# Optimization experiments

Measured on AMD Instinct MI355X. Metric: run time of the kernel, lower is better.

Reference implementation:

```python
import jax, jax.numpy as jnp
import numpy as np

B, L, E = 8, 2048, 128


def setup_inputs() -> dict:
    key = jax.random.key(0)
    k1, k2, k3, k4 = jax.random.split(key, 4)
    return {
        "Uq": jax.random.normal(k1, (B, L, E), dtype=jnp.float32),
        "Uid": jax.random.normal(k2, (B, L, E), dtype=jnp.float32),
        "mask": jnp.ones((L, L), dtype=jnp.float32),
        "Wc_w": jax.random.normal(k3, (3 * E,), dtype=jnp.float32) * 0.05,
        "Wc_b": jax.random.normal(k4, (), dtype=jnp.float32) * 0.05,
    }


def reference(Uq, Uid, mask, Wc_w, Wc_b):
    # Wc(cat(Uid, Uq, Uid*Uq)) decomposed into three direct projections —
    # exact same math as the Linear over the concatenation, never
    # materializing the [B, L, L, 3E] tensor.
    e = Uq.shape[-1]
    w_id, w_q, w_mul = Wc_w[:e], Wc_w[e:2 * e], Wc_w[2 * e:]
    s_id = jnp.einsum("bie,e->bi", Uid, w_id)          # [B, Lid]
    s_q = jnp.einsum("bje,e->bj", Uq, w_q)             # [B, Lq]
    s_mul = jnp.einsum("bie,bje,e->bij", Uid, Uq, w_mul)  # [B, Lid, Lq]
    S = (s_id[:, :, None] + s_q[:, None, :] + s_mul + Wc_b) * mask
    # S_D2Q = Softmax(dim=0) over the per-example [Lid, Lq] matrix -> axis=1
    P = jax.nn.softmax(S, axis=1)                      # [B, Lid, Lq]
    A_D2Q = jnp.einsum("bij,bje->bie", P, Uq)          # [B, Lid, E]
    M = jnp.einsum("bij,bkj->bik", P, P)               # P @ P^T, [B, Lid, Lid]
    A_Q2D = jnp.einsum("bik,bke->bie", M, Uid)         # [B, Lid, E]
    Vid = jnp.concatenate([Uid, A_D2Q, Uid * A_D2Q, Uid * A_Q2D], axis=-1)
    return Vid  # [B, Lid, 4E]
```

## Files before the change

kernel.cpp:

```cpp
#include <hip/hip_runtime.h>

#define L 2048
#define E 128
#define NB 8

typedef float f32x4 __attribute__((ext_vector_type(4)));
typedef short short8 __attribute__((ext_vector_type(8)));
typedef unsigned int u32;

static __device__ inline float bf2f(ushort u) {
  union { float f; u32 i; } v; v.i = ((u32)u) << 16; return v.f;
}
static __device__ inline ushort f2bf(float f) {
  union { float f; u32 i; } v; v.f = f;
  u32 x = v.i;
  return (ushort)((x + 0x7fffu + ((x >> 16) & 1u)) >> 16);
}

__device__ inline void glds16(const ushort* g, ushort* l) {
  __builtin_amdgcn_global_load_lds(
      (const __attribute__((address_space(1))) u32*)(const void*)g,
      (__attribute__((address_space(3))) u32*)(void*)l, 16, 0, 0);
}

__global__ __launch_bounds__(128) void k_prep(const float* __restrict__ Uq,
                                              const float* __restrict__ Uid,
                                              const float* __restrict__ Wcw,
                                              ushort* __restrict__ UqB,
                                              ushort* __restrict__ UidB,
                                              ushort* __restrict__ Uidw,
                                              float* __restrict__ s_id,
                                              float* __restrict__ s_q) {
  int r = blockIdx.x;
  int e = threadIdx.x;
  ushort uqu  = f2bf(Uq[(long)r * E + e]);
  ushort uidu = f2bf(Uid[(long)r * E + e]);
  float uqf = bf2f(uqu), uidf = bf2f(uidu);
  float wid  = bf2f(f2bf(Wcw[e]));
  float wq   = bf2f(f2bf(Wcw[E + e]));
  float wmul = bf2f(f2bf(Wcw[2 * E + e]));
  UqB[(long)r * E + e]  = uqu;
  UidB[(long)r * E + e] = uidu;
  Uidw[(long)r * E + e] = f2bf(uidf * wmul);
  float sid = uidf * wid, sq = uqf * wq;
  #pragma unroll
  for (int off = 32; off >= 1; off >>= 1) {
    sid += __shfl_down(sid, off, 64);
    sq  += __shfl_down(sq,  off, 64);
  }
  __shared__ float red[4];
  int wv = threadIdx.x >> 6;
  if ((threadIdx.x & 63) == 0) { red[wv * 2] = sid; red[wv * 2 + 1] = sq; }
  __syncthreads();
  if (threadIdx.x == 0) { s_id[r] = red[0] + red[2]; s_q[r] = red[1] + red[3]; }
}

__global__ __launch_bounds__(256) void k_maskT(const float* __restrict__ mask,
                                               ushort* __restrict__ maskT) {
  __shared__ ushort tile[32][33];
  int j0 = blockIdx.x * 32, i0 = blockIdx.y * 32;
  int tx = threadIdx.x, ty = threadIdx.y;
  #pragma unroll
  for (int r = ty; r < 32; r += 8)
    tile[r][tx] = f2bf(mask[(long)(i0 + r) * L + j0 + tx]);
  __syncthreads();
  #pragma unroll
  for (int r = ty; r < 32; r += 8)
    maskT[(long)(j0 + r) * L + i0 + tx] = tile[tx][r];
}

__global__ __launch_bounds__(256) void k_tr2(const ushort* __restrict__ s1,
                                             ushort* __restrict__ d1,
                                             const ushort* __restrict__ s2,
                                             ushort* __restrict__ d2) {
  __shared__ ushort tile[32][33];
  int zz = blockIdx.z;
  long base = (long)(zz & (NB - 1)) * L * E;
  const ushort* src = ((zz < NB) ? s1 : s2) + base;
  ushort* dst = ((zz < NB) ? d1 : d2) + base;
  int c0 = blockIdx.x * 32, r0 = blockIdx.y * 32;
  int tx = threadIdx.x, ty = threadIdx.y;
  #pragma unroll
  for (int i = ty; i < 32; i += 8)
    tile[i][tx] = src[(long)(r0 + i) * E + c0 + tx];
  __syncthreads();
  #pragma unroll
  for (int i = ty; i < 32; i += 8)
    dst[(long)(c0 + i) * L + r0 + tx] = tile[tx][i];
}

__device__ inline void gemm128_loop(const ushort* __restrict__ A,
                                    const ushort* __restrict__ B,
                                    long ldA, long ldB, int K,
                                    f32x4 acc[4][4],
                                    ushort* ldsA, ushort* ldsB) {
  const int t = threadIdx.x;
  const int w = t >> 6, lane = t & 63;
  const int mrow = lane & 15, quad = lane >> 4;
  const int lr = lane >> 3;
  const int lc = ((lane & 7) ^ lr) * 8;
  const int mh = (w & 1) * 64, nh = (w >> 1) * 64;
  for (int k0 = 0; k0 < K; k0 += 64) {
    __syncthreads();
    #pragma unroll
    for (int s = 0; s < 4; s++) {
      int row = w * 32 + s * 8 + lr;
      glds16(&A[(long)row * ldA + k0 + lc], &ldsA[w * 2048 + s * 512]);
      glds16(&B[(long)row * ldB + k0 + lc], &ldsB[w * 2048 + s * 512]);
    }
    __syncthreads();
    #pragma unroll
    for (int kk = 0; kk < 2; kk++) {
      short8 av[4], bv[4];
      #pragma unroll
      for (int mi = 0; mi < 4; mi++)
        av[mi] = *(const short8*)&ldsA[(mh + mi * 16 + mrow) * 64 +
                                       ((kk * 32 + quad * 8) ^ ((mrow & 7) << 3))];
      #pragma unroll
      for (int ni = 0; ni < 4; ni++)
        bv[ni] = *(const short8*)&ldsB[(nh + ni * 16 + mrow) * 64 +
                                       ((kk * 32 + quad * 8) ^ ((mrow & 7) << 3))];
      #pragma unroll
      for (int mi = 0; mi < 4; mi++)
        #pragma unroll
        for (int ni = 0; ni < 4; ni++)
          acc[mi][ni] = __builtin_amdgcn_mfma_f32_16x16x32_bf16(av[mi], bv[ni], acc[mi][ni], 0, 0, 0);
    }
  }
}

__device__ inline void gemm64x64_dbuf(const ushort* __restrict__ A,
                                      const ushort* __restrict__ B,
                                      long ldA, long ldB, int K,
                                      f32x4 acc[2][2],
                                      ushort* ldsA, ushort* ldsB) {
  const int t = threadIdx.x;
  const int w = t >> 6, lane = t & 63;
  const int mrow = lane & 15, quad = lane >> 4;
  const int lr = lane >> 3;
  const int lc = ((lane & 7) ^ lr) * 8;
  const int mh = (w & 1) * 32, nh = (w >> 1) * 32;
  #pragma unroll
  for (int s = 0; s < 2; s++) {
    int row = w * 16 + s * 8 + lr;
    glds16(&A[(long)row * ldA + lc], &ldsA[w * 1024 + s * 512]);
    glds16(&B[(long)row * ldB + lc], &ldsB[w * 1024 + s * 512]);
  }
  int cur = 0;
  for (int k0 = 0; k0 < K; k0 += 64) {
    __syncthreads();
    int nxt = cur ^ 1;
    if (k0 + 64 < K) {
      #pragma unroll
      for (int s = 0; s < 2; s++) {
        int row = w * 16 + s * 8 + lr;
        glds16(&A[(long)row * ldA + k0 + 64 + lc], &ldsA[nxt * 4096 + w * 1024 + s * 512]);
        glds16(&B[(long)row * ldB + k0 + 64 + lc], &ldsB[nxt * 4096 + w * 1024 + s * 512]);
      }
    }
    const ushort* cA = &ldsA[cur * 4096];
    const ushort* cB = &ldsB[cur * 4096];
    #pragma unroll
    for (int kk = 0; kk < 2; kk++) {
      short8 av[2], bv[2];
      #pragma unroll
      for (int mi = 0; mi < 2; mi++)
        av[mi] = *(const short8*)&cA[(mh + mi * 16 + mrow) * 64 +
                                     ((kk * 32 + quad * 8) ^ ((mrow & 7) << 3))];
      #pragma unroll
      for (int ni = 0; ni < 2; ni++)
        bv[ni] = *(const short8*)&cB[(nh + ni * 16 + mrow) * 64 +
                                     ((kk * 32 + quad * 8) ^ ((mrow & 7) << 3))];
      #pragma unroll
      for (int mi = 0; mi < 2; mi++)
        #pragma unroll
        for (int ni = 0; ni < 2; ni++)
          acc[mi][ni] = __builtin_amdgcn_mfma_f32_16x16x32_bf16(av[mi], bv[ni], acc[mi][ni], 0, 0, 0);
    }
    cur = nxt;
  }
}

__global__ __launch_bounds__(256) void k_scores(const ushort* __restrict__ Uq,
                                                const ushort* __restrict__ Uidw,
                                                const float* __restrict__ s_id,
                                                const float* __restrict__ s_q,
                                                const float* __restrict__ Wcb,
                                                const ushort* __restrict__ maskT,
                                                ushort* __restrict__ St,
                                                float* __restrict__ ps, int b0) {
  __shared__ ushort lds[16384];
  ushort* ldsA = lds;
  ushort* ldsB = lds + 8192;
  int bz = blockIdx.z, b = b0 + bz;
  int m0 = blockIdx.x * 128;
  int n0 = blockIdx.y * 128;
  int tile_i = blockIdx.y;
  const ushort* A = Uq   + (long)b * L * E + (long)m0 * E;
  const ushort* B = Uidw + (long)b * L * E + (long)n0 * E;
  f32x4 acc[4][4] = {};
  gemm128_loop(A, B, E, E, E, acc, ldsA, ldsB);
  float bias = bf2f(f2bf(Wcb[0]));
  const int t = threadIdx.x, w = t >> 6, lane = t & 63;
  const int col = lane & 15, quad = lane >> 4;
  const int mh = (w & 1) * 64, nh = (w >> 1) * 64;

  __syncthreads();
  float sidv[4];
  #pragma unroll
  for (int ni = 0; ni < 4; ni++)
    sidv[ni] = s_id[b * L + n0 + nh + ni * 16 + col];
  #pragma unroll
  for (int mi = 0; mi < 4; mi++) {
    float sqv[4];
    #pragma unroll
    for (int rg = 0; rg < 4; rg++)
      sqv[rg] = s_q[b * L + m0 + mh + mi * 16 + quad * 4 + rg];
    #pragma unroll
    for (int ni = 0; ni < 4; ni++) {
      int cl = nh + ni * 16 + col;
      #pragma unroll
      for (int rg = 0; rg < 4; rg++) {
        int row = mh + mi * 16 + quad * 4 + rg;
        float v = acc[mi][ni][rg] + sqv[rg] + sidv[ni] + bias;
        lds[row * 128 + (cl ^ ((row & 7) << 3))] = f2bf(v);
      }
    }
  }
  __syncthreads();
  ushort oall[64];
  #pragma unroll
  for (int p = 0; p < 8; p++) {
    int r2 = p * 16 + (t >> 4);
    int cu = (t & 15) * 8;
    uint4 sv = *(const uint4*)&lds[r2 * 128 + (cu ^ ((r2 & 7) << 3))];
    int jg = m0 + r2;
    uint4 mv = *(const uint4*)&maskT[(long)jg * L + n0 + cu];
    float lsum = 0.f;
    const ushort* sp = (const ushort*)&sv;
    const ushort* mp = (const ushort*)&mv;
    #pragma unroll
    for (int k = 0; k < 8; k++) {
      float ev = __expf(bf2f(sp[k]) * bf2f(mp[k]));
      oall[p * 8 + k] = f2bf(ev);
      lsum += bf2f(oall[p * 8 + k]);
    }
    #pragma unroll
    for (int off = 8; off >= 1; off >>= 1) lsum += __shfl_xor(lsum, off, 64);
    if ((t & 15) == 0) {
      ps[((long)bz * L + jg) * 16 + tile_i] = lsum;
    }
  }
  #pragma unroll
  for (int p = 0; p < 8; p++) {
    int r2 = p * 16 + (t >> 4);
    int cu = (t & 15) * 8;
    int jg = m0 + r2;
    *(uint4*)&St[(long)bz * L * L + (long)jg * L + n0 + cu] = *(const uint4*)&oall[p * 8];
  }
}

__global__ __launch_bounds__(256) void k_redstats(const float* __restrict__ ps,
                                                  float* __restrict__ lg) {
  int idx = blockIdx.x * 256 + threadIdx.x;
  const float* psr = ps + (long)idx * 16;
  float s = 0.f;
  #pragma unroll
  for (int k = 0; k < 16; k++) s += psr[k];
  lg[idx] = 1.0f / s;
}

__global__ __launch_bounds__(256) void k_gemm_Tt(const ushort* __restrict__ UidT,
                                                 const ushort* __restrict__ Et,
                                                 const float* __restrict__ lg,
                                                 ushort* __restrict__ Tt, int b0) {
  __shared__ ushort lds[16384];
  ushort* ldsA = lds;
  ushort* ldsB = lds + 8192;
  int bz = blockIdx.z, b = b0 + bz;
  int e0 = (blockIdx.x & 1) * 64;
  int j0 = (blockIdx.x >> 1) * 64;
  const ushort* A = UidT + (long)b * E * L + (long)e0 * L;
  const ushort* B = Et   + (long)bz * L * L + (long)j0 * L;
  f32x4 acc[2][2] = {};
  gemm64x64_dbuf(A, B, L, L, L, acc, ldsA, ldsB);
  const int t = threadIdx.x, w = t >> 6, lane = t & 63;
  const int col = lane & 15, quad = lane >> 4;
  const int mh = (w & 1) * 32, nh = (w >> 1) * 32;
  __syncthreads();
  #pragma unroll
  for (int mi = 0; mi < 2; mi++)
    #pragma unroll
    for (int ni = 0; ni < 2; ni++) {
      int cl = nh + ni * 16 + col;
      float sc = lg[(long)bz * L + j0 + cl];
      #pragma unroll
      for (int rg = 0; rg < 4; rg++) {
        int row = mh + mi * 16 + quad * 4 + rg;
        lds[row * 64 + (cl ^ ((row & 7) << 3))] = f2bf(acc[mi][ni][rg] * sc);
      }
    }
  __syncthreads();
  #pragma unroll
  for (int p = 0; p < 2; p++) {
    int r2 = p * 32 + (t >> 3);
    int cu = (t & 7) * 8;
    uint4 v = *(const uint4*)&lds[r2 * 64 + (cu ^ ((r2 & 7) << 3))];
    *(uint4*)&Tt[(long)b * E * L + (long)(e0 + r2) * L + j0 + cu] = v;
  }
}

__global__ __launch_bounds__(512) void k_gemm_A(const ushort* __restrict__ Et,
                                                const ushort* __restrict__ UqT,
                                                const ushort* __restrict__ Tt,
                                                const ushort* __restrict__ UidB,
                                                const float* __restrict__ lg,
                                                float* __restrict__ out, int b0) {
  __shared__ ushort ldsA[2 * 4608];
  __shared__ ushort ldsB[2 * 8192];
  int bz = blockIdx.z, b = b0 + bz;
  int m0 = blockIdx.x * 64;
  int n0 = blockIdx.y * 128;
  const ushort* Eb = Et + (long)bz * L * L + m0;
  const float* lgb = lg + (long)bz * L;
  const ushort* B = (blockIdx.y == 0) ? (UqT + (long)b * E * L)
                                      : (Tt  + (long)b * E * L);
  const int t = threadIdx.x, w = t >> 6, lane = t & 63;
  const int mrow = lane & 15, quad = lane >> 4;
  const int lr = lane >> 3;
  const int lc = ((lane & 7) ^ lr) * 8;
  const int mh = (w & 1) * 32, nh = (w >> 1) * 32;
  const int jp2 = (t >> 4) * 2;
  const int ic  = (t & 15) * 4;
  f32x4 acc[2][2] = {};
  uint2 q0 = *(const uint2*)&Eb[(long)jp2 * L + ic];
  uint2 q1 = *(const uint2*)&Eb[(long)(jp2 + 1) * L + ic];
  float s0 = lgb[jp2], s1 = lgb[jp2 + 1];
  #pragma unroll
  for (int s = 0; s < 2; s++) {
    int row = w * 16 + s * 8 + lr;
    glds16(&B[(long)row * L + lc], &ldsB[w * 1024 + s * 512]);
  }
  {
    const ushort* p0 = (const ushort*)&q0;
    const ushort* p1 = (const ushort*)&q1;
    #pragma unroll
    for (int k = 0; k < 4; k++) {
      u32 pk = (u32)f2bf(bf2f(p0[k]) * s0) |
               ((u32)f2bf(bf2f(p1[k]) * s1) << 16);
      int i = ic + k;
      int cs = jp2 ^ (((i >> 3) & 7) << 3);
      *(u32*)&ldsA[i * 72 + cs] = pk;
    }
  }
  q0 = *(const uint2*)&Eb[(long)(64 + jp2) * L + ic];
  q1 = *(const uint2*)&Eb[(long)(64 + jp2 + 1) * L + ic];
  s0 = lgb[64 + jp2]; s1 = lgb[64 + jp2 + 1];

  int cur = 0;
  for (int k0 = 0; k0 < L; k0 += 64) {
    __syncthreads();
    int nxt = cur ^ 1;
    if (k0 + 64 < L) {
      #pragma unroll
      for (int s = 0; s < 2; s++) {
        int row = w * 16 + s * 8 + lr;
        glds16(&B[(long)row * L + k0 + 64 + lc], &ldsB[nxt * 8192 + w * 1024 + s * 512]);
      }
      const ushort* p0 = (const ushort*)&q0;
      const ushort* p1 = (const ushort*)&q1;
      #pragma unroll
      for (int k = 0; k < 4; k++) {
        u32 pk = (u32)f2bf(bf2f(p0[k]) * s0) |
                 ((u32)f2bf(bf2f(p1[k]) * s1) << 16);
        int i = ic + k;
        int cs = jp2 ^ (((i >> 3) & 7) << 3);
        *(u32*)&ldsA[nxt * 4608 + i * 72 + cs] = pk;
      }
    }
    if (k0 + 128 < L) {
      q0 = *(const uint2*)&Eb[(long)(k0 + 128 + jp2) * L + ic];
      q1 = *(const uint2*)&Eb[(long)(k0 + 128 + jp2 + 1) * L + ic];
      s0 = lgb[k0 + 128 + jp2]; s1 = lgb[k0 + 128 + jp2 + 1];
    }
    const ushort* cA = &ldsA[cur * 4608];
    const ushort* cB = &ldsB[cur * 8192];
    #pragma unroll
    for (int kk = 0; kk < 2; kk++) {
      short8 av[2], bv[2];
      #pragma unroll
      for (int mi = 0; mi < 2; mi++) {
        int i = mh + mi * 16 + mrow;
        av[mi] = *(const short8*)&cA[i * 72 +
                   ((kk * 32 + quad * 8) ^ (((i >> 3) & 7) << 3))];
      }
      #pragma unroll
      for (int ni = 0; ni < 2; ni++)
        bv[ni] = *(const short8*)&cB[(nh + ni * 16 + mrow) * 64 +
                                     ((kk * 32 + quad * 8) ^ ((mrow & 7) << 3))];
      #pragma unroll
      for (int mi = 0; mi < 2; mi++)
        #pragma unroll
        for (int ni = 0; ni < 2; ni++)
          acc[mi][ni] = __builtin_amdgcn_mfma_f32_16x16x32_bf16(av[mi], bv[ni], acc[mi][ni], 0, 0, 0);
    }
    cur = nxt;
  }
  const int col = mrow;
  #pragma unroll
  for (int mi = 0; mi < 2; mi++)
    #pragma unroll
    for (int ni = 0; ni < 2; ni++)
      #pragma unroll
      for (int rg = 0; rg < 4; rg++) {
        int ig = m0 + mh + mi * 16 + quad * 4 + rg;
        int c  = n0 + nh + ni * 16 + col;
        float a = acc[mi][ni][rg];
        float uidf = bf2f(UidB[(long)b * L * E + (long)ig * E + (c & 127)]);
        long ob = ((long)b * L + ig) * 512;
        if (c < 128) {
          out[ob + c]       = uidf;
          out[ob + 128 + c] = a;
          out[ob + 256 + c] = uidf * a;
        } else {
          out[ob + 256 + c] = uidf * a;
        }
      }
}

extern "C" void kernel_launch(void* const* d_in, const int* in_sizes, int n_in,
                              void* d_out, int out_size, void* d_ws, size_t ws_size,
                              hipStream_t stream) {
  const float* Uq   = (const float*)d_in[0];
  const float* Uid  = (const float*)d_in[1];
  const float* mask = (const float*)d_in[2];
  const float* Wcw  = (const float*)d_in[3];
  const float* Wcb  = (const float*)d_in[4];
  float* out = (float*)d_out;

  char* ws = (char*)d_ws;
  size_t off = 0;
  auto alloc = [&](size_t bytes) -> void* {
    void* p = ws + off; off += (bytes + 255) & ~(size_t)255; return p;
  };
  const size_t nUb = (size_t)NB * L * E * 2;
  ushort* UqB   = (ushort*)alloc(nUb);
  ushort* UidB  = (ushort*)alloc(nUb);
  ushort* Uidw  = (ushort*)alloc(nUb);
  ushort* UqT   = (ushort*)alloc(nUb);
  ushort* UidT  = (ushort*)alloc(nUb);
  ushort* Tt    = (ushort*)alloc(nUb);
  ushort* maskT = (ushort*)alloc((size_t)L * L * 2);
  float*  s_id  = (float*)alloc((size_t)NB * L * 4);
  float*  s_q   = (float*)alloc((size_t)NB * L * 4);
  float*  lg    = (float*)alloc((size_t)NB * L * 4);
  float*  ps    = (float*)alloc((size_t)NB * L * 16 * 4);
  const size_t per_batch = (size_t)L * L * 2;
  size_t avail = (ws_size > off + per_batch) ? (ws_size - off) : per_batch;
  int nb_c = (int)(avail / per_batch);
  if (nb_c < 1) nb_c = 1;
  if (nb_c > NB) nb_c = NB;
  ushort* St = (ushort*)(ws + off);

  dim3 tb(32, 8);
  k_prep<<<NB * L, E, 0, stream>>>(Uq, Uid, Wcw, UqB, UidB, Uidw, s_id, s_q);
  k_maskT<<<dim3(L / 32, L / 32), tb, 0, stream>>>(mask, maskT);
  k_tr2<<<dim3(E / 32, L / 32, 2 * NB), tb, 0, stream>>>(UqB, UqT, UidB, UidT);

  for (int b0 = 0; b0 < NB; b0 += nb_c) {
    int nb = (NB - b0 < nb_c) ? (NB - b0) : nb_c;
    k_scores<<<dim3(L / 128, L / 128, nb), 256, 0, stream>>>(UqB, Uidw, s_id, s_q, Wcb, maskT, St, ps, b0);
    k_redstats<<<dim3(nb * L / 256), 256, 0, stream>>>(ps, lg);
    k_gemm_Tt<<<dim3(2 * (L / 64), 1, nb), 256, 0, stream>>>(UidT, St, lg, Tt, b0);
    k_gemm_A<<<dim3(L / 64, 2, nb), 512, 0, stream>>>(St, UqT, Tt, UidB, lg, out, b0);
  }
}
```

Baseline: 203.9 us.

## Fuse transposes into vectorized prep kernel and widen score tiles to 128x256

```diff
diff --git a/kernel.cpp b/kernel.cpp
--- a/kernel.cpp
+++ b/kernel.cpp
@@ -23,36 +23,75 @@
       (__attribute__((address_space(3))) u32*)(void*)l, 16, 0, 0);
 }
 
-__global__ __launch_bounds__(128) void k_prep(const float* __restrict__ Uq,
-                                              const float* __restrict__ Uid,
-                                              const float* __restrict__ Wcw,
-                                              ushort* __restrict__ UqB,
-                                              ushort* __restrict__ UidB,
-                                              ushort* __restrict__ Uidw,
-                                              float* __restrict__ s_id,
-                                              float* __restrict__ s_q) {
-  int r = blockIdx.x;
-  int e = threadIdx.x;
-  ushort uqu  = f2bf(Uq[(long)r * E + e]);
-  ushort uidu = f2bf(Uid[(long)r * E + e]);
-  float uqf = bf2f(uqu), uidf = bf2f(uidu);
-  float wid  = bf2f(f2bf(Wcw[e]));
-  float wq   = bf2f(f2bf(Wcw[E + e]));
-  float wmul = bf2f(f2bf(Wcw[2 * E + e]));
-  UqB[(long)r * E + e]  = uqu;
-  UidB[(long)r * E + e] = uidu;
-  Uidw[(long)r * E + e] = f2bf(uidf * wmul);
-  float sid = uidf * wid, sq = uqf * wq;
-  #pragma unroll
-  for (int off = 32; off >= 1; off >>= 1) {
-    sid += __shfl_down(sid, off, 64);
-    sq  += __shfl_down(sq,  off, 64);
-  }
-  __shared__ float red[4];
-  int wv = threadIdx.x >> 6;
-  if ((threadIdx.x & 63) == 0) { red[wv * 2] = sid; red[wv * 2 + 1] = sq; }
+__global__ __launch_bounds__(512) void k_prep2(const float* __restrict__ Uq,
+                                               const float* __restrict__ Uid,
+                                               const float* __restrict__ Wcw,
+                                               ushort* __restrict__ UqB,
+                                               ushort* __restrict__ UidB,
+                                               ushort* __restrict__ Uidw,
+                                               ushort* __restrict__ UqT,
+                                               ushort* __restrict__ UidT,
+                                               float* __restrict__ s_id,
+                                               float* __restrict__ s_q) {
+  __shared__ float ldsW[384];
+  __shared__ ushort tq[128 * 72];
+  __shared__ ushort td[128 * 72];
+  int t = threadIdx.x;
+  if (t < 384) ldsW[t] = bf2f(f2bf(Wcw[t]));
+  long r0 = (long)blockIdx.x * 64;
+  int r = t >> 3;
+  int e0 = (t & 7) * 16;
   __syncthreads();
-  if (threadIdx.x == 0) { s_id[r] = red[0] + red[2]; s_q[r] = red[1] + red[3]; }
+  const float* pq = Uq  + (r0 + r) * E + e0;
+  const float* pd = Uid + (r0 + r) * E + e0;
+  float4 q4[4], d4[4];
+  #pragma unroll
+  for (int c = 0; c < 4; c++) { q4[c] = *(const float4*)(pq + c * 4); d4[c] = *(const float4*)(pd + c * 4); }
+  ushort uqb[16], udb[16], uwb[16];
+  float sid = 0.f, sq = 0.f;
+  #pragma unroll
+  for (int c = 0; c < 4; c++) {
+    const float* qf4 = (const float*)&q4[c];
+    const float* df4 = (const float*)&d4[c];
+    #pragma unroll
+    for (int j = 0; j < 4; j++) {
+      int k = c * 4 + j;
+      ushort qb = f2bf(qf4[j]), db = f2bf(df4[j]);
+      float qf = bf2f(qb), df = bf2f(db);
+      uqb[k] = qb; udb[k] = db;
+      uwb[k] = f2bf(df * ldsW[256 + e0 + k]);
+      sid += df * ldsW[e0 + k];
+      sq  += qf * ldsW[128 + e0 + k];
+    }
+  }
+  long rb = (r0 + r) * E + e0;
+  *(uint4*)&UqB[rb]      = *(const uint4*)&uqb[0];
+  *(uint4*)&UqB[rb + 8]  = *(const uint4*)&uqb[8];
+  *(uint4*)&UidB[rb]     = *(const uint4*)&udb[0];
+  *(uint4*)&UidB[rb + 8] = *(const uint4*)&udb[8];
+  *(uint4*)&Uidw[rb]     = *(const uint4*)&uwb[0];
+  *(uint4*)&Uidw[rb + 8] = *(const uint4*)&uwb[8];
+  #pragma unroll
+  for (int off = 4; off >= 1; off >>= 1) {
+    sid += __shfl_xor(sid, off, 64);
+    sq  += __shfl_xor(sq,  off, 64);
+  }
+  if ((t & 7) == 0) { s_id[r0 + r] = sid; s_q[r0 + r] = sq; }
+  #pragma unroll
+  for (int k = 0; k < 16; k++) {
+    tq[(e0 + k) * 72 + r] = uqb[k];
+    td[(e0 + k) * 72 + r] = udb[k];
+  }
+  __syncthreads();
+  int e = t >> 2, rs = (t & 3) * 16;
+  long b = r0 / L, rl = r0 - b * L;
+  long ob = b * E * L + (long)e * L + rl + rs;
+  uint4 v0 = *(const uint4*)&tq[e * 72 + rs];
+  uint4 v1 = *(const uint4*)&tq[e * 72 + rs + 8];
+  *(uint4*)&UqT[ob] = v0; *(uint4*)&UqT[ob + 8] = v1;
+  v0 = *(const uint4*)&td[e * 72 + rs];
+  v1 = *(const uint4*)&td[e * 72 + rs + 8];
+  *(uint4*)&UidT[ob] = v0; *(uint4*)&UidT[ob + 8] = v1;
 }
 
 __global__ __launch_bounds__(256) void k_maskT(const float* __restrict__ mask,
@@ -69,44 +108,41 @@
     maskT[(long)(j0 + r) * L + i0 + tx] = tile[tx][r];
 }
 
-__global__ __launch_bounds__(256) void k_tr2(const ushort* __restrict__ s1,
-                                             ushort* __restrict__ d1,
-                                             const ushort* __restrict__ s2,
-                                             ushort* __restrict__ d2) {
-  __shared__ ushort tile[32][33];
-  int zz = blockIdx.z;
-  long base = (long)(zz & (NB - 1)) * L * E;
-  const ushort* src = ((zz < NB) ? s1 : s2) + base;
-  ushort* dst = ((zz < NB) ? d1 : d2) + base;
-  int c0 = blockIdx.x * 32, r0 = blockIdx.y * 32;
-  int tx = threadIdx.x, ty = threadIdx.y;
-  #pragma unroll
-  for (int i = ty; i < 32; i += 8)
-    tile[i][tx] = src[(long)(r0 + i) * E + c0 + tx];
-  __syncthreads();
-  #pragma unroll
-  for (int i = ty; i < 32; i += 8)
-    dst[(long)(c0 + i) * L + r0 + tx] = tile[tx][i];
-}
-
-__device__ inline void gemm128_loop(const ushort* __restrict__ A,
-                                    const ushort* __restrict__ B,
-                                    long ldA, long ldB, int K,
-                                    f32x4 acc[4][4],
-                                    ushort* ldsA, ushort* ldsB) {
-  const int t = threadIdx.x;
-  const int w = t >> 6, lane = t & 63;
+__global__ __launch_bounds__(512) void k_scores(const ushort* __restrict__ Uq,
+                                                const ushort* __restrict__ Uidw,
+                                                const float* __restrict__ s_id,
+                                                const float* __restrict__ s_q,
+                                                const float* __restrict__ Wcb,
+                                                const ushort* __restrict__ maskT,
+                                                ushort* __restrict__ St,
+                                                float* __restrict__ ps, int b0) {
+  __shared__ ushort lds[24576];
+  ushort* ldsA = lds;
+  ushort* ldsB = lds + 8192;
+  int bz = blockIdx.z, b = b0 + bz;
+  int m0 = blockIdx.x * 128;
+  int n0 = blockIdx.y * 256;
+  int tile_i = blockIdx.y;
+  const ushort* A = Uq   + (long)b * L * E + (long)m0 * E;
+  const ushort* B = Uidw + (long)b * L * E + (long)n0 * E;
+  const int t = threadIdx.x, w = t >> 6, lane = t & 63;
   const int mrow = lane & 15, quad = lane >> 4;
   const int lr = lane >> 3;
   const int lc = ((lane & 7) ^ lr) * 8;
-  const int mh = (w & 1) * 64, nh = (w >> 1) * 64;
-  for (int k0 = 0; k0 < K; k0 += 64) {
-    __syncthreads();
+  const int mh = (w & 1) * 64;
+  const int nh2 = (w >> 1);
+  f32x4 acc[4][4] = {};
+  for (int k0 = 0; k0 < E; k0 += 64) {
+    __syncthreads();
+    #pragma unroll
+    for (int s = 0; s < 2; s++) {
+      int row = w * 16 + s * 8 + lr;
+      glds16(&A[(long)row * E + k0 + lc], &ldsA[w * 1024 + s * 512]);
+    }
     #pragma unroll
     for (int s = 0; s < 4; s++) {
       int row = w * 32 + s * 8 + lr;
-      glds16(&A[(long)row * ldA + k0 + lc], &ldsA[w * 2048 + s * 512]);
-      glds16(&B[(long)row * ldB + k0 + lc], &ldsB[w * 2048 + s * 512]);
+      glds16(&B[(long)row * E + k0 + lc], &ldsB[w * 2048 + s * 512]);
     }
     __syncthreads();
     #pragma unroll
@@ -118,7 +154,7 @@
                                        ((kk * 32 + quad * 8) ^ ((mrow & 7) << 3))];
       #pragma unroll
       for (int ni = 0; ni < 4; ni++)
-        bv[ni] = *(const short8*)&ldsB[(nh + ni * 16 + mrow) * 64 +
+        bv[ni] = *(const short8*)&ldsB[(nh2 * 64 + ni * 16 + mrow) * 64 +
                                        ((kk * 32 + quad * 8) ^ ((mrow & 7) << 3))];
       #pragma unroll
       for (int mi = 0; mi < 4; mi++)
@@ -127,6 +163,75 @@
           acc[mi][ni] = __builtin_amdgcn_mfma_f32_16x16x32_bf16(av[mi], bv[ni], acc[mi][ni], 0, 0, 0);
     }
   }
+  float bias = bf2f(f2bf(Wcb[0]));
+  const int col = mrow;
+  for (int h = 0; h < 2; h++) {
+    __syncthreads();
+    if ((w >> 2) == h) {
+      int nl = (nh2 & 1) * 64;
+      float sidv[4];
+      #pragma unroll
+      for (int ni = 0; ni < 4; ni++)
+        sidv[ni] = s_id[b * L + n0 + h * 128 + nl + ni * 16 + col];
+      #pragma unroll
+      for (int mi = 0; mi < 4; mi++) {
+        float sqv[4];
+        #pragma unroll
+        for (int rg = 0; rg < 4; rg++)
+          sqv[rg] = s_q[b * L + m0 + mh + mi * 16 + quad * 4 + rg];
+        #pragma unroll
+        for (int ni = 0; ni < 4; ni++) {
+          int cl = nl + ni * 16 + col;
+          #pragma unroll
+          for (int rg = 0; rg < 4; rg++) {
+            int row = mh + mi * 16 + quad * 4 + rg;
+            float v = acc[mi][ni][rg] + sqv[rg] + sidv[ni] + bias;
+            lds[row * 128 + (cl ^ ((row & 7) << 3))] = f2bf(v);
+          }
+        }
+      }
+    }
+    __syncthreads();
+    ushort oall[32];
+    #pragma unroll
+    for (int p = 0; p < 4; p++) {
+      int r2 = p * 32 + (t >> 4);
+      int cu = (t & 15) * 8;
+      uint4 sv = *(const uint4*)&lds[r2 * 128 + (cu ^ ((r2 & 7) << 3))];
+      int jg = m0 + r2;
+      uint4 mv = *(const uint4*)&maskT[(long)jg * L + n0 + h * 128 + cu];
+      float lsum = 0.f;
+      const ushort* sp = (const ushort*)&sv;
+      const ushort* mp = (const ushort*)&mv;
+      #pragma unroll
+      for (int k = 0; k < 8; k++) {
+        float ev = __expf(bf2f(sp[k]) * bf2f(mp[k]));
+        oall[p * 8 + k] = f2bf(ev);
+        lsum += bf2f(oall[p * 8 + k]);
+      }
+      #pragma unroll
+      for (int off = 8; off >= 1; off >>= 1) lsum += __shfl_xor(lsum, off, 64);
+      if ((t & 15) == 0)
+        ps[((long)bz * L + jg) * 16 + tile_i * 2 + h] = lsum;
+    }
+    #pragma unroll
+    for (int p = 0; p < 4; p++) {
+      int r2 = p * 32 + (t >> 4);
+      int cu = (t & 15) * 8;
+      int jg = m0 + r2;
+      *(uint4*)&St[(long)bz * L * L + (long)jg * L + n0 + h * 128 + cu] = *(const uint4*)&oall[p * 8];
+    }
+  }
+}
+
+__global__ __launch_bounds__(256) void k_redstats(const float* __restrict__ ps,
+                                                  float* __restrict__ lg) {
+  int idx = blockIdx.x * 256 + threadIdx.x;
+  const float* psr = ps + (long)idx * 16;
+  float s = 0.f;
+  #pragma unroll
+  for (int k = 0; k < 16; k++) s += psr[k];
+  lg[idx] = 1.0f / s;
 }
 
 __device__ inline void gemm64x64_dbuf(const ushort* __restrict__ A,
@@ -179,95 +284,6 @@
     }
     cur = nxt;
   }
-}
-
-__global__ __launch_bounds__(256) void k_scores(const ushort* __restrict__ Uq,
-                                                const ushort* __restrict__ Uidw,
-                                                const float* __restrict__ s_id,
-                                                const float* __restrict__ s_q,
-                                                const float* __restrict__ Wcb,
-                                                const ushort* __restrict__ maskT,
-                                                ushort* __restrict__ St,
-                                                float* __restrict__ ps, int b0) {
-  __shared__ ushort lds[16384];
-  ushort* ldsA = lds;
-  ushort* ldsB = lds + 8192;
-  int bz = blockIdx.z, b = b0 + bz;
-  int m0 = blockIdx.x * 128;
-  int n0 = blockIdx.y * 128;
-  int tile_i = blockIdx.y;
-  const ushort* A = Uq   + (long)b * L * E + (long)m0 * E;
-  const ushort* B = Uidw + (long)b * L * E + (long)n0 * E;
-  f32x4 acc[4][4] = {};
-  gemm128_loop(A, B, E, E, E, acc, ldsA, ldsB);
-  float bias = bf2f(f2bf(Wcb[0]));
-  const int t = threadIdx.x, w = t >> 6, lane = t & 63;
-  const int col = lane & 15, quad = lane >> 4;
-  const int mh = (w & 1) * 64, nh = (w >> 1) * 64;
-
-  __syncthreads();
-  float sidv[4];
-  #pragma unroll
-  for (int ni = 0; ni < 4; ni++)
-    sidv[ni] = s_id[b * L + n0 + nh + ni * 16 + col];
-  #pragma unroll
-  for (int mi = 0; mi < 4; mi++) {
-    float sqv[4];
-    #pragma unroll
-    for (int rg = 0; rg < 4; rg++)
-      sqv[rg] = s_q[b * L + m0 + mh + mi * 16 + quad * 4 + rg];
-    #pragma unroll
-    for (int ni = 0; ni < 4; ni++) {
-      int cl = nh + ni * 16 + col;
-      #pragma unroll
-      for (int rg = 0; rg < 4; rg++) {
-        int row = mh + mi * 16 + quad * 4 + rg;
-        float v = acc[mi][ni][rg] + sqv[rg] + sidv[ni] + bias;
-        lds[row * 128 + (cl ^ ((row & 7) << 3))] = f2bf(v);
-      }
-    }
-  }
-  __syncthreads();
-  ushort oall[64];
-  #pragma unroll
-  for (int p = 0; p < 8; p++) {
-    int r2 = p * 16 + (t >> 4);
-    int cu = (t & 15) * 8;
-    uint4 sv = *(const uint4*)&lds[r2 * 128 + (cu ^ ((r2 & 7) << 3))];
-    int jg = m0 + r2;
-    uint4 mv = *(const uint4*)&maskT[(long)jg * L + n0 + cu];
-    float lsum = 0.f;
-    const ushort* sp = (const ushort*)&sv;
-    const ushort* mp = (const ushort*)&mv;
-    #pragma unroll
-    for (int k = 0; k < 8; k++) {
-      float ev = __expf(bf2f(sp[k]) * bf2f(mp[k]));
-      oall[p * 8 + k] = f2bf(ev);
-      lsum += bf2f(oall[p * 8 + k]);
-    }
-    #pragma unroll
-    for (int off = 8; off >= 1; off >>= 1) lsum += __shfl_xor(lsum, off, 64);
-    if ((t & 15) == 0) {
-      ps[((long)bz * L + jg) * 16 + tile_i] = lsum;
-    }
-  }
-  #pragma unroll
-  for (int p = 0; p < 8; p++) {
-    int r2 = p * 16 + (t >> 4);
-    int cu = (t & 15) * 8;
-    int jg = m0 + r2;
-    *(uint4*)&St[(long)bz * L * L + (long)jg * L + n0 + cu] = *(const uint4*)&oall[p * 8];
-  }
-}
-
-__global__ __launch_bounds__(256) void k_redstats(const float* __restrict__ ps,
-                                                  float* __restrict__ lg) {
-  int idx = blockIdx.x * 256 + threadIdx.x;
-  const float* psr = ps + (long)idx * 16;
-  float s = 0.f;
-  #pragma unroll
-  for (int k = 0; k < 16; k++) s += psr[k];
-  lg[idx] = 1.0f / s;
 }
 
 __global__ __launch_bounds__(256) void k_gemm_Tt(const ushort* __restrict__ UidT,
@@ -463,13 +479,12 @@
   ushort* St = (ushort*)(ws + off);
 
   dim3 tb(32, 8);
-  k_prep<<<NB * L, E, 0, stream>>>(Uq, Uid, Wcw, UqB, UidB, Uidw, s_id, s_q);
+  k_prep2<<<NB * L / 64, 512, 0, stream>>>(Uq, Uid, Wcw, UqB, UidB, Uidw, UqT, UidT, s_id, s_q);
   k_maskT<<<dim3(L / 32, L / 32), tb, 0, stream>>>(mask, maskT);
-  k_tr2<<<dim3(E / 32, L / 32, 2 * NB), tb, 0, stream>>>(UqB, UqT, UidB, UidT);
 
   for (int b0 = 0; b0 < NB; b0 += nb_c) {
     int nb = (NB - b0 < nb_c) ? (NB - b0) : nb_c;
-    k_scores<<<dim3(L / 128, L / 128, nb), 256, 0, stream>>>(UqB, Uidw, s_id, s_q, Wcb, maskT, St, ps, b0);
+    k_scores<<<dim3(L / 128, L / 256, nb), 512, 0, stream>>>(UqB, Uidw, s_id, s_q, Wcb, maskT, St, ps, b0);
     k_redstats<<<dim3(nb * L / 256), 256, 0, stream>>>(ps, lg);
     k_gemm_Tt<<<dim3(2 * (L / 64), 1, nb), 256, 0, stream>>>(UidT, St, lg, Tt, b0);
     k_gemm_A<<<dim3(L / 64, 2, nb), 512, 0, stream>>>(St, UqT, Tt, UidB, lg, out, b0);
```

Measured after the change: 208.1 us. 1.02x slower.
